# Kernel tuning notes

Measured on AMD Instinct MI355X. Metric: run time of the kernel, lower is better.

The kernel has to match this reference:

```python
import jax, jax.numpy as jnp
import numpy as np

TEMP = 0.02
B, T, V, E, H, D = 128, 128, 10000, 256, 1024, 128


def setup_inputs() -> dict:
    key = jax.random.key(0)
    ks = jax.random.split(key, 8)
    s = 0.05  # small init scale for numerical stability
    return {
        "tokens": jax.random.randint(ks[0], (B, T), 0, V),
        "emb": jax.random.normal(ks[1], (V, E), jnp.float32) * s,
        "gru_k": jax.random.normal(ks[2], (E, 3 * H), jnp.float32) * s,
        "gru_rk": jax.random.normal(ks[3], (H, 3 * H), jnp.float32) * s,
        "gru_bi": jax.random.normal(ks[4], (3 * H,), jnp.float32) * s,
        "gru_br": jax.random.normal(ks[5], (3 * H,), jnp.float32) * s,
        "w1": jax.random.normal(ks[6], (H, D), jnp.float32) * s,
        "b1": jnp.zeros((D,), jnp.float32),
        "w2": jax.random.normal(ks[7], (D, V), jnp.float32) * s,
        "b2": jnp.zeros((V,), jnp.float32),
    }


def _gru_scan(xg, gru_rk, gru_br, h0):
    # xg: [T, B, 3H] precomputed input-side gate activations (incl. input bias)
    # Keras GRU with reset_after=True: reset gate applied AFTER recurrent matmul,
    # separate recurrent bias.
    def step(h, xt):
        rg = jnp.dot(h, gru_rk) + gru_br            # [B, 3H]
        xz, xr, xh = jnp.split(xt, 3, axis=-1)
        rz, rr, rh = jnp.split(rg, 3, axis=-1)
        z = jax.nn.sigmoid(xz + rz)
        r = jax.nn.sigmoid(xr + rr)
        hh = jnp.tanh(xh + r * rh)
        hn = z * h + (1.0 - z) * hh
        return hn, hn

    return jax.lax.scan(step, h0, xg)


def reference(tokens, emb, gru_k, gru_rk, gru_bi, gru_br, w1, b1, w2, b2):
    x = emb[tokens]                                  # [B, T, E]
    xg = jnp.einsum('bte,eg->btg', x, gru_k) + gru_bi  # [B, T, 3H]
    xg = jnp.transpose(xg, (1, 0, 2))                # [T, B, 3H]
    h0 = jnp.zeros((tokens.shape[0], gru_rk.shape[0]), x.dtype)
    _, hs = _gru_scan(xg, gru_rk, gru_br, h0)        # [T, B, H]
    hs = jnp.transpose(hs, (1, 0, 2))                # [B, T, H]
    d = jax.nn.relu(jnp.dot(hs, w1) + b1)            # [B, T, D]
    logits = jnp.dot(d, w2) + b2                     # [B, T, V]
    return jax.nn.softmax(logits / TEMP, axis=-1)
```

## Files before the change

### kernel.cpp

```cpp
#include <hip/hip_runtime.h>
#include <cstdint>
#include <cstddef>

#define B_   128
#define T_   128
#define V_   10000
#define E_   256
#define H_   1024
#define D_   128
#define G3_  3072
#define GRID_ 256

__device__ __forceinline__ float sigmoid_(float x) {
  return 1.0f / (1.0f + __expf(-x));
}

__global__ void bar_reset(unsigned int* bar) { *bar = 0u; }

__global__ __launch_bounds__(256, 1) void gru_all(
    const int* __restrict__ tokens, const float* __restrict__ emb,
    const float* __restrict__ gk, const float* __restrict__ rk,
    const float* __restrict__ bi, const float* __restrict__ br,
    float* __restrict__ hs, unsigned int* __restrict__ bar) {
  __shared__ float wT[3][4][H_];
  __shared__ float gT[3][4][E_];
  __shared__ unsigned short tok16[128][T_];
  __shared__ float a_lds[128][72];
  __shared__ float hn_lds[128][4];

  const int tid = threadIdx.x;
  const int b_lo = tid & 63;
  const int j_idx = tid >> 6;
  const int j0 = blockIdx.x << 2;
  const int j = j0 + j_idx;
  const int lk = tid & 63;
  const int lb0 = tid >> 6;

  for (int i = tid; i < H_ * 3; i += 256) {
    int k = i / 3, g = i - 3 * k;
    float4 v = *(const float4*)&rk[(size_t)k * G3_ + (g << 10) + j0];
    wT[g][0][k] = v.x; wT[g][1][k] = v.y; wT[g][2][k] = v.z; wT[g][3][k] = v.w;
  }
  for (int i = tid; i < E_ * 3; i += 256) {
    int k = i / 3, g = i - 3 * k;
    float4 v = *(const float4*)&gk[(size_t)k * G3_ + (g << 10) + j0];
    gT[g][0][k] = v.x; gT[g][1][k] = v.y; gT[g][2][k] = v.z; gT[g][3][k] = v.w;
  }
  for (int i = tid; i < B_ * T_; i += 256)
    tok16[i >> 7][i & (T_ - 1)] = (unsigned short)tokens[i];

  const float bi_z = bi[j], bi_r = bi[H_ + j], bi_h = bi[2 * H_ + j];
  const float br_z = br[j], br_r = br[H_ + j], br_h = br[2 * H_ + j];

  float hp0 = 0.f, hp1 = 0.f;

  for (int t = 0; t < T_; ++t) {
    float xz0 = 0.f, xr0 = 0.f, xh0 = 0.f, xz1 = 0.f, xr1 = 0.f, xh1 = 0.f;
    float hz0 = 0.f, hr0 = 0.f, hh0 = 0.f, hz1 = 0.f, hh1 = 0.f, hr1 = 0.f;

    for (int ec = 0; ec < E_; ec += 64) {
      __syncthreads();
      #pragma unroll
      for (int i = 0; i < 32; ++i) {
        int b = lb0 + (i << 2);
        a_lds[b][lk] = emb[(size_t)tok16[b][t] * E_ + ec + lk];
      }
      __syncthreads();
      for (int k = 0; k < 64; k += 4) {
        float a0v[4], a1v[4], wz[4], wr[4], wh[4];
        *(float4*)a0v = *(const float4*)&a_lds[b_lo][k];
        *(float4*)a1v = *(const float4*)&a_lds[b_lo + 64][k];
        *(float4*)wz = *(const float4*)&gT[0][j_idx][ec + k];
        *(float4*)wr = *(const float4*)&gT[1][j_idx][ec + k];
        *(float4*)wh = *(const float4*)&gT[2][j_idx][ec + k];
        #pragma unroll
        for (int u = 0; u < 4; ++u) {
          xz0 = fmaf(a0v[u], wz[u], xz0);
          xr0 = fmaf(a0v[u], wr[u], xr0);
          xh0 = fmaf(a0v[u], wh[u], xh0);
          xz1 = fmaf(a1v[u], wz[u], xz1);
          xr1 = fmaf(a1v[u], wr[u], xr1);
          xh1 = fmaf(a1v[u], wh[u], xh1);
        }
      }
    }

    if (t > 0) {
      if (tid == 0) {
        const unsigned int tgt = (unsigned)GRID_ * (unsigned)t;
        while (__hip_atomic_load(bar, __ATOMIC_RELAXED,
                                 __HIP_MEMORY_SCOPE_AGENT) < tgt)
          __builtin_amdgcn_s_sleep(2);
        __threadfence();
      }
      __syncthreads();

      const float* __restrict__ hprev = hs + (size_t)(t - 1) * (B_ * H_);
      for (int kc = 0; kc < H_; kc += 64) {
        __syncthreads();
        #pragma unroll
        for (int i = 0; i < 32; ++i) {
          int b = lb0 + (i << 2);
          a_lds[b][lk] = hprev[(size_t)b * H_ + kc + lk];
        }
        __syncthreads();
        for (int k = 0; k < 64; k += 4) {
          float a0v[4], a1v[4], wz[4], wr[4], wh[4];
          *(float4*)a0v = *(const float4*)&a_lds[b_lo][k];
          *(float4*)a1v = *(const float4*)&a_lds[b_lo + 64][k];
          *(float4*)wz = *(const float4*)&wT[0][j_idx][kc + k];
          *(float4*)wr = *(const float4*)&wT[1][j_idx][kc + k];
          *(float4*)wh = *(const float4*)&wT[2][j_idx][kc + k];
          #pragma unroll
          for (int u = 0; u < 4; ++u) {
            hz0 = fmaf(a0v[u], wz[u], hz0);
            hr0 = fmaf(a0v[u], wr[u], hr0);
            hh0 = fmaf(a0v[u], wh[u], hh0);
            hz1 = fmaf(a1v[u], wz[u], hz1);
            hr1 = fmaf(a1v[u], wr[u], hr1);
            hh1 = fmaf(a1v[u], wh[u], hh1);
          }
        }
      }
    }

    float z0 = sigmoid_(xz0 + bi_z + hz0 + br_z);
    float r0 = sigmoid_(xr0 + bi_r + hr0 + br_r);
    float c0 = tanhf(xh0 + bi_h + r0 * (hh0 + br_h));
    float hn0 = z0 * hp0 + (1.f - z0) * c0;

    float z1 = sigmoid_(xz1 + bi_z + hz1 + br_z);
    float r1 = sigmoid_(xr1 + bi_r + hr1 + br_r);
    float c1 = tanhf(xh1 + bi_h + r1 * (hh1 + br_h));
    float hn1 = z1 * hp1 + (1.f - z1) * c1;

    hp0 = hn0; hp1 = hn1;

    hn_lds[b_lo][j_idx] = hn0;
    hn_lds[b_lo + 64][j_idx] = hn1;
    __syncthreads();
    if (tid < 128) {
      float4 v = *(const float4*)&hn_lds[tid][0];
      *(float4*)&hs[((size_t)t * B_ + tid) * H_ + j0] = v;
    }
    __syncthreads();

    if (t + 1 < T_ && tid == 0) {
      __threadfence();
      __hip_atomic_fetch_add(bar, 1u, __ATOMIC_RELEASE,
                             __HIP_MEMORY_SCOPE_AGENT);
    }
  }
}

__global__ __launch_bounds__(256) void mlp1_kernel(
    const float* __restrict__ hs, const float* __restrict__ w1,
    const float* __restrict__ b1, float* __restrict__ dbuf) {
  __shared__ float A[64][68];
  __shared__ float Bs[64][128];
  const int tid = threadIdx.x;
  const int row0 = blockIdx.x * 64;
  const int tc = tid & 15;
  const int tr = tid >> 4;

  float acc[4][8];
  #pragma unroll
  for (int i = 0; i < 4; ++i)
    #pragma unroll
    for (int u = 0; u < 8; ++u) acc[i][u] = 0.f;

  const int lk = tid & 63, lr0 = tid >> 6;
  const int lc = tid & 127, lk0 = tid >> 7;

  for (int kc = 0; kc < H_; kc += 64) {
    __syncthreads();
    #pragma unroll
    for (int i = 0; i < 16; ++i) {
      int r = lr0 + (i << 2);
      A[r][lk] = hs[(size_t)(row0 + r) * H_ + kc + lk];
    }
    #pragma unroll
    for (int i = 0; i < 32; ++i) {
      int k = lk0 + (i << 1);
      Bs[k][lc] = w1[(size_t)(kc + k) * D_ + lc];
    }
    __syncthreads();
    for (int k = 0; k < 64; ++k) {
      float av[4];
      #pragma unroll
      for (int i = 0; i < 4; ++i) av[i] = A[(tr << 2) + i][k];
      float bv[8];
      *(float4*)&bv[0] = *(const float4*)&Bs[k][tc * 8];
      *(float4*)&bv[4] = *(const float4*)&Bs[k][tc * 8 + 4];
      #pragma unroll
      for (int i = 0; i < 4; ++i)
        #pragma unroll
        for (int u = 0; u < 8; ++u) acc[i][u] = fmaf(av[i], bv[u], acc[i][u]);
    }
  }

  float bb[8];
  #pragma unroll
  for (int u = 0; u < 8; ++u) bb[u] = b1[tc * 8 + u];
  #pragma unroll
  for (int i = 0; i < 4; ++i) {
    int row = row0 + (tr << 2) + i;
    float o[8];
    #pragma unroll
    for (int u = 0; u < 8; ++u) o[u] = fmaxf(acc[i][u] + bb[u], 0.f);
    *(float4*)&dbuf[(size_t)row * D_ + tc * 8] = *(float4*)&o[0];
    *(float4*)&dbuf[(size_t)row * D_ + tc * 8 + 4] = *(float4*)&o[4];
  }
}

__global__ __launch_bounds__(256) void mlp2_logits(
    const float* __restrict__ dbuf, const float* __restrict__ w2,
    const float* __restrict__ b2, float* __restrict__ out) {
  __shared__ float A[64][68];
  __shared__ float Bs[64][128];
  const int tid = threadIdx.x;
  const int col0 = blockIdx.x * 128;
  const int row0 = blockIdx.y * 64;
  const int tc = tid & 15;
  const int tr = tid >> 4;

  float acc[4][8];
  #pragma unroll
  for (int i = 0; i < 4; ++i)
    #pragma unroll
    for (int u = 0; u < 8; ++u) acc[i][u] = 0.f;

  const int lk = tid & 63, lr0 = tid >> 6;
  const int lc = tid & 127, lk0 = tid >> 7;

  for (int kc = 0; kc < D_; kc += 64) {
    __syncthreads();
    #pragma unroll
    for (int i = 0; i < 16; ++i) {
      int r = lr0 + (i << 2);
      A[r][lk] = dbuf[(size_t)(row0 + r) * D_ + kc + lk];
    }
    #pragma unroll
    for (int i = 0; i < 32; ++i) {
      int k = lk0 + (i << 1);
      int col = col0 + lc;
      Bs[k][lc] = (col < V_) ? w2[(size_t)(kc + k) * V_ + col] : 0.f;
    }
    __syncthreads();
    for (int k = 0; k < 64; ++k) {
      float av[4];
      #pragma unroll
      for (int i = 0; i < 4; ++i) av[i] = A[(tr << 2) + i][k];
      float bv[8];
      *(float4*)&bv[0] = *(const float4*)&Bs[k][tc * 8];
      *(float4*)&bv[4] = *(const float4*)&Bs[k][tc * 8 + 4];
      #pragma unroll
      for (int i = 0; i < 4; ++i)
        #pragma unroll
        for (int u = 0; u < 8; ++u) acc[i][u] = fmaf(av[i], bv[u], acc[i][u]);
    }
  }

  const int colg = col0 + tc * 8;
  if (colg < V_) {
    float bb[8];
    #pragma unroll
    for (int u = 0; u < 8; ++u) bb[u] = b2[colg + u];
    #pragma unroll
    for (int i = 0; i < 4; ++i) {
      int row = row0 + (tr << 2) + i;
      int b = row & (B_ - 1);
      int tt = row >> 7;
      size_t base = ((size_t)b * T_ + tt) * V_ + colg;
      float o[8];
      #pragma unroll
      for (int u = 0; u < 8; ++u) o[u] = acc[i][u] + bb[u];
      *(float4*)&out[base] = *(float4*)&o[0];
      *(float4*)&out[base + 4] = *(float4*)&o[4];
    }
  }
}

__global__ __launch_bounds__(256) void softmax_rows(float* __restrict__ out) {
  __shared__ float buf[V_];
  __shared__ float red[8];
  const int tid = threadIdx.x;
  const size_t base = (size_t)blockIdx.x * V_;

  float m = -1e30f;
  for (int i = tid; i < V_; i += 256) {
    float v = out[base + i];
    buf[i] = v;
    m = fmaxf(m, v);
  }
  #pragma unroll
  for (int o = 32; o > 0; o >>= 1) m = fmaxf(m, __shfl_down(m, o));
  if ((tid & 63) == 0) red[tid >> 6] = m;
  __syncthreads();
  if (tid == 0) red[4] = fmaxf(fmaxf(red[0], red[1]), fmaxf(red[2], red[3]));
  __syncthreads();
  const float mall = red[4];

  float s = 0.f;
  for (int i = tid; i < V_; i += 256) {
    float e = __expf((buf[i] - mall) * 50.0f);
    buf[i] = e;
    s += e;
  }
  #pragma unroll
  for (int o = 32; o > 0; o >>= 1) s += __shfl_down(s, o);
  if ((tid & 63) == 0) red[tid >> 6] = s;
  __syncthreads();
  if (tid == 0) red[5] = red[0] + red[1] + red[2] + red[3];
  __syncthreads();
  const float inv = 1.0f / red[5];

  for (int i = tid; i < V_; i += 256) out[base + i] = buf[i] * inv;
}

extern "C" void kernel_launch(void* const* d_in, const int* in_sizes, int n_in,
                              void* d_out, int out_size, void* d_ws, size_t ws_size,
                              hipStream_t stream) {
  const int*   tokens = (const int*)d_in[0];
  const float* emb    = (const float*)d_in[1];
  const float* gru_k  = (const float*)d_in[2];
  const float* gru_rk = (const float*)d_in[3];
  const float* gru_bi = (const float*)d_in[4];
  const float* gru_br = (const float*)d_in[5];
  const float* w1     = (const float*)d_in[6];
  const float* b1     = (const float*)d_in[7];
  const float* w2     = (const float*)d_in[8];
  const float* b2     = (const float*)d_in[9];
  float* out = (float*)d_out;

  float* ws  = (float*)d_ws;
  float* hs  = ws;
  float* dbf = hs + (size_t)T_ * B_ * H_;
  unsigned int* bar = (unsigned int*)dbf;

  bar_reset<<<1, 1, 0, stream>>>(bar);
  gru_all<<<GRID_, 256, 0, stream>>>(tokens, emb, gru_k, gru_rk,
                                     gru_bi, gru_br, hs, bar);
  mlp1_kernel<<<256, 256, 0, stream>>>(hs, w1, b1, dbf);
  mlp2_logits<<<dim3((V_ + 127) / 128, (T_ * B_) / 64), 256, 0, stream>>>(
      dbf, w2, b2, out);
  softmax_rows<<<T_ * B_, 256, 0, stream>>>(out);
}
```

Baseline: 9.959 ms.

## Double-buffer GRU operand tiles with register prefetch and XOR-swizzled LDS layout

Restructures the per-step embedding and recurrent-state loads in the persistent GRU kernel into a double-buffered pipeline. The next 64-wide chunk is fetched into registers as float4s while the current chunk is consumed from LDS, and the last embedding chunk is overlapped with the first recurrent chunk after the grid barrier. The LDS tile becomes unpadded with an XOR swizzle to avoid bank conflicts, and each chunk now needs one barrier instead of two. This costs extra registers for staging and a second LDS buffer.

Result: slower. 19.84 ms (+99.2%).

```diff
diff --git a/kernel.cpp b/kernel.cpp
--- a/kernel.cpp
+++ b/kernel.cpp
@@ -17,24 +17,78 @@
 
 __global__ void bar_reset(unsigned int* bar) { *bar = 0u; }
 
+__device__ __forceinline__ void ld_emb(float4 (&stg)[8], const float* __restrict__ emb,
+                                       const unsigned short (*tok16)[T_], int t,
+                                       int ec, int cg, int rr) {
+  #pragma unroll
+  for (int i = 0; i < 8; ++i) {
+    int r = rr + (i << 4);
+    stg[i] = *(const float4*)&emb[(size_t)tok16[r][t] * E_ + ec + (cg << 2)];
+  }
+}
+
+__device__ __forceinline__ void ld_rec(float4 (&stg)[8], const float* __restrict__ hprev,
+                                       int kc, int cg, int rr) {
+  #pragma unroll
+  for (int i = 0; i < 8; ++i) {
+    int r = rr + (i << 4);
+    stg[i] = *(const float4*)&hprev[(size_t)r * H_ + kc + (cg << 2)];
+  }
+}
+
+__device__ __forceinline__ void st_tile(const float4 (&stg)[8], float (*buf)[64],
+                                        int cg, int rr) {
+  #pragma unroll
+  for (int i = 0; i < 8; ++i) {
+    int r = rr + (i << 4);
+    *(float4*)&buf[r][(cg ^ (r & 15)) << 2] = stg[i];
+  }
+}
+
+template <int KD>
+__device__ __forceinline__ void chunk_fma(
+    const float (*buf)[64], const float (&W)[3][4][KD], int ko,
+    int b_lo, int bm, int j_idx,
+    float& z0, float& r0, float& h0, float& z1, float& r1, float& h1) {
+  #pragma unroll
+  for (int kk = 0; kk < 16; ++kk) {
+    float a0v[4], a1v[4], wz[4], wr[4], wh[4];
+    *(float4*)a0v = *(const float4*)&buf[b_lo][(kk ^ bm) << 2];
+    *(float4*)a1v = *(const float4*)&buf[b_lo + 64][(kk ^ bm) << 2];
+    *(float4*)wz = *(const float4*)&W[0][j_idx][ko + (kk << 2)];
+    *(float4*)wr = *(const float4*)&W[1][j_idx][ko + (kk << 2)];
+    *(float4*)wh = *(const float4*)&W[2][j_idx][ko + (kk << 2)];
+    #pragma unroll
+    for (int u = 0; u < 4; ++u) {
+      z0 = fmaf(a0v[u], wz[u], z0);
+      r0 = fmaf(a0v[u], wr[u], r0);
+      h0 = fmaf(a0v[u], wh[u], h0);
+      z1 = fmaf(a1v[u], wz[u], z1);
+      r1 = fmaf(a1v[u], wr[u], r1);
+      h1 = fmaf(a1v[u], wh[u], h1);
+    }
+  }
+}
+
 __global__ __launch_bounds__(256, 1) void gru_all(
     const int* __restrict__ tokens, const float* __restrict__ emb,
     const float* __restrict__ gk, const float* __restrict__ rk,
     const float* __restrict__ bi, const float* __restrict__ br,
     float* __restrict__ hs, unsigned int* __restrict__ bar) {
-  __shared__ float wT[3][4][H_];
-  __shared__ float gT[3][4][E_];
+  __shared__ __align__(16) float wT[3][4][H_];
+  __shared__ __align__(16) float gT[3][4][E_];
   __shared__ unsigned short tok16[128][T_];
-  __shared__ float a_lds[128][72];
-  __shared__ float hn_lds[128][4];
+  __shared__ __align__(16) float a_lds[2][128][64];
+  __shared__ __align__(16) float hn_lds[128][4];
 
   const int tid = threadIdx.x;
   const int b_lo = tid & 63;
   const int j_idx = tid >> 6;
   const int j0 = blockIdx.x << 2;
   const int j = j0 + j_idx;
-  const int lk = tid & 63;
-  const int lb0 = tid >> 6;
+  const int cg = tid & 15;
+  const int rr = tid >> 4;
+  const int bm = b_lo & 15;
 
   for (int i = tid; i < H_ * 3; i += 256) {
     int k = i / 3, g = i - 3 * k;
@@ -48,6 +102,7 @@
   }
   for (int i = tid; i < B_ * T_; i += 256)
     tok16[i >> 7][i & (T_ - 1)] = (unsigned short)tokens[i];
+  __syncthreads();
 
   const float bi_z = bi[j], bi_r = bi[H_ + j], bi_h = bi[2 * H_ + j];
   const float br_z = br[j], br_r = br[H_ + j], br_h = br[2 * H_ + j];
@@ -56,33 +111,28 @@
 
   for (int t = 0; t < T_; ++t) {
     float xz0 = 0.f, xr0 = 0.f, xh0 = 0.f, xz1 = 0.f, xr1 = 0.f, xh1 = 0.f;
-    float hz0 = 0.f, hr0 = 0.f, hh0 = 0.f, hz1 = 0.f, hh1 = 0.f, hr1 = 0.f;
-
-    for (int ec = 0; ec < E_; ec += 64) {
+    float hz0 = 0.f, hr0 = 0.f, hh0 = 0.f, hz1 = 0.f, hr1 = 0.f, hh1 = 0.f;
+
+    const float* __restrict__ hprev = hs + (size_t)(t - 1) * (B_ * H_);
+
+    float (*cur)[64] = a_lds[0];
+    float (*nxt)[64] = a_lds[1];
+
+    {
+      float4 stg[8];
+      ld_emb(stg, emb, tok16, t, 0, cg, rr);
+      st_tile(stg, cur, cg, rr);
+    }
+    __syncthreads();
+
+    for (int c = 0; c < 3; ++c) {
+      float4 stg[8];
+      ld_emb(stg, emb, tok16, t, (c + 1) << 6, cg, rr);
+      chunk_fma<E_>(cur, gT, c << 6, b_lo, bm, j_idx,
+                    xz0, xr0, xh0, xz1, xr1, xh1);
+      st_tile(stg, nxt, cg, rr);
       __syncthreads();
-      #pragma unroll
-      for (int i = 0; i < 32; ++i) {
-        int b = lb0 + (i << 2);
-        a_lds[b][lk] = emb[(size_t)tok16[b][t] * E_ + ec + lk];
-      }
-      __syncthreads();
-      for (int k = 0; k < 64; k += 4) {
-        float a0v[4], a1v[4], wz[4], wr[4], wh[4];
-        *(float4*)a0v = *(const float4*)&a_lds[b_lo][k];
-        *(float4*)a1v = *(const float4*)&a_lds[b_lo + 64][k];
-        *(float4*)wz = *(const float4*)&gT[0][j_idx][ec + k];
-        *(float4*)wr = *(const float4*)&gT[1][j_idx][ec + k];
-        *(float4*)wh = *(const float4*)&gT[2][j_idx][ec + k];
-        #pragma unroll
-        for (int u = 0; u < 4; ++u) {
-          xz0 = fmaf(a0v[u], wz[u], xz0);
-          xr0 = fmaf(a0v[u], wr[u], xr0);
-          xh0 = fmaf(a0v[u], wh[u], xh0);
-          xz1 = fmaf(a1v[u], wz[u], xz1);
-          xr1 = fmaf(a1v[u], wr[u], xr1);
-          xh1 = fmaf(a1v[u], wh[u], xh1);
-        }
-      }
+      float (*tmp)[64] = cur; cur = nxt; nxt = tmp;
     }
 
     if (t > 0) {
@@ -94,33 +144,27 @@
         __threadfence();
       }
       __syncthreads();
-
-      const float* __restrict__ hprev = hs + (size_t)(t - 1) * (B_ * H_);
-      for (int kc = 0; kc < H_; kc += 64) {
+    }
+
+    {
+      float4 stg[8];
+      if (t > 0) ld_rec(stg, hprev, 0, cg, rr);
+      chunk_fma<E_>(cur, gT, 192, b_lo, bm, j_idx,
+                    xz0, xr0, xh0, xz1, xr1, xh1);
+      if (t > 0) st_tile(stg, nxt, cg, rr);
+      __syncthreads();
+      float (*tmp)[64] = cur; cur = nxt; nxt = tmp;
+    }
+
+    if (t > 0) {
+      for (int c = 0; c < 16; ++c) {
+        float4 stg[8];
+        if (c < 15) ld_rec(stg, hprev, (c + 1) << 6, cg, rr);
+        chunk_fma<H_>(cur, wT, c << 6, b_lo, bm, j_idx,
+                      hz0, hr0, hh0, hz1, hr1, hh1);
+        if (c < 15) st_tile(stg, nxt, cg, rr);
         __syncthreads();
-        #pragma unroll
-        for (int i = 0; i < 32; ++i) {
-          int b = lb0 + (i << 2);
-          a_lds[b][lk] = hprev[(size_t)b * H_ + kc + lk];
-        }
-        __syncthreads();
-        for (int k = 0; k < 64; k += 4) {
-          float a0v[4], a1v[4], wz[4], wr[4], wh[4];
-          *(float4*)a0v = *(const float4*)&a_lds[b_lo][k];
-          *(float4*)a1v = *(const float4*)&a_lds[b_lo + 64][k];
-          *(float4*)wz = *(const float4*)&wT[0][j_idx][kc + k];
-          *(float4*)wr = *(const float4*)&wT[1][j_idx][kc + k];
-          *(float4*)wh = *(const float4*)&wT[2][j_idx][kc + k];
-          #pragma unroll
-          for (int u = 0; u < 4; ++u) {
-            hz0 = fmaf(a0v[u], wz[u], hz0);
-            hr0 = fmaf(a0v[u], wr[u], hr0);
-            hh0 = fmaf(a0v[u], wh[u], hh0);
-            hz1 = fmaf(a1v[u], wz[u], hz1);
-            hr1 = fmaf(a1v[u], wr[u], hr1);
-            hh1 = fmaf(a1v[u], wh[u], hh1);
-          }
-        }
+        float (*tmp)[64] = cur; cur = nxt; nxt = tmp;
       }
     }
 
```
